# Kernel optimization log

Measured on AMD Instinct MI355X. Metric: run time of the kernel, lower is better.

Reference implementation:

```python
import jax, jax.numpy as jnp
import numpy as np

B, L, H, E = 4, 2048, 8, 64
S, D = L, E

def setup_inputs() -> dict:
    key = jax.random.key(0)
    kq, kk, kv = jax.random.split(key, 3)
    queries = jax.random.normal(kq, (B, L, H, E), dtype=jnp.float32)
    keys = jax.random.normal(kk, (B, S, H, E), dtype=jnp.float32)
    values = jax.random.normal(kv, (B, S, H, D), dtype=jnp.float32)
    # TriangularCausalMask: True above the diagonal -> masked out
    attn_mask = jnp.broadcast_to(
        jnp.triu(jnp.ones((L, S), dtype=bool), k=1)[None, None], (B, 1, L, S)
    )
    return {"queries": queries, "keys": keys, "values": values, "attn_mask": attn_mask}

def reference(queries, keys, values, attn_mask):
    E_ = queries.shape[-1]
    scale = 1.0 / jnp.sqrt(jnp.float32(E_))
    # scores: [B, H, L, S]
    scores = jnp.einsum('blhe,bshe->bhls', queries, keys)
    scores = jnp.where(attn_mask, -jnp.inf, scores)
    A = jax.nn.softmax(scale * scores, axis=-1)  # dropout p=0.01 omitted (eval/deterministic)
    V = jnp.einsum('bhls,bshd->blhd', A, values)
    return (V, A)
```

## Files before the change

kernel.cpp:

```cpp
#include <hip/hip_runtime.h>
#include <hip/hip_bf16.h>
#include <stdint.h>
#include <stddef.h>

typedef __bf16 bf16;
typedef __attribute__((ext_vector_type(8))) __bf16 bf16x8;
typedef __attribute__((ext_vector_type(4))) float f32x4;
typedef unsigned short u16;
typedef __attribute__((ext_vector_type(4))) u16 u16x4;

#define NB 4
#define NL 2048
#define NH 8
#define NE 64
#define NS 2048
#define ND 64
#define CM 0.18033688011112042f
#define STR 72

__device__ __forceinline__ void barrier_keep_vm() {
    asm volatile("s_waitcnt lgkmcnt(0)" ::: "memory");
    __builtin_amdgcn_s_barrier();
    asm volatile("" ::: "memory");
}

__global__ __launch_bounds__(512, 4)
void attn_fwd(const float* __restrict__ Qg, const float* __restrict__ Kg,
              const float* __restrict__ Vg, float* __restrict__ Og,
              float* __restrict__ Ag)
{
    __shared__ __attribute__((aligned(16))) bf16 Kl[2][64 * STR];
    __shared__ __attribute__((aligned(16))) bf16 Vl[2][64 * STR];
    __shared__ __attribute__((aligned(16))) bf16 Pl[8][16 * STR];

    const int bid = blockIdx.x;
    const int x   = bid & 7;
    const int u   = bid >> 3;
    const int qb  = (u < 32) ? (u & 15) : 15 - (u & 15);
    const int bh  = x * 4 + (u >> 4);
    const int b   = bh >> 3;
    const int h   = bh & 7;
    const int q0  = qb * 128;
    const int jmax = 2 * qb + 1;

    const int tid  = threadIdx.x;
    const int wid  = tid >> 6;
    const int lane = tid & 63;
    const int g    = lane >> 4;
    const int li   = lane & 15;
    const int jd   = 2 * qb + (wid >> 2);

    const float* qp = Qg + (((size_t)b * NL + q0 + wid * 16 + li) * NH + h) * NE;
    bf16x8 qf[2];
#pragma unroll
    for (int t = 0; t < 2; ++t) {
        f32x4 x0 = *(const f32x4*)(qp + t * 32 + g * 8);
        f32x4 x1 = *(const f32x4*)(qp + t * 32 + g * 8 + 4);
        bf16x8 v;
#pragma unroll
        for (int e = 0; e < 4; ++e) { v[e] = (bf16)x0[e]; v[4 + e] = (bf16)x1[e]; }
        qf[t] = v;
    }

    float* Abase = Ag + (((size_t)(b * NH + h)) * NL + q0) * NS;

    const int srow = tid >> 3;
    const int scb  = (tid & 7) * 8;
    const float* kbase = Kg + (((size_t)b * NS + srow) * NH + h) * NE + scb;
    const float* vbase = Vg + (((size_t)b * NS + srow) * NH + h) * ND + scb;

    auto loadK = [&](int j, f32x4 r[2]) {
        const float* src = kbase + (size_t)j * 64 * NH * NE;
        r[0] = *(const f32x4*)(src);
        r[1] = *(const f32x4*)(src + 4);
    };
    auto loadV = [&](int j, f32x4 r[2]) {
        const float* src = vbase + (size_t)j * 64 * NH * ND;
        r[0] = *(const f32x4*)(src);
        r[1] = *(const f32x4*)(src + 4);
    };
    auto writeK = [&](int c, const f32x4 r[2]) {
        bf16x8 w;
#pragma unroll
        for (int e = 0; e < 4; ++e) { w[e] = (bf16)r[0][e]; w[4 + e] = (bf16)r[1][e]; }
        *(bf16x8*)(Kl[c] + srow * STR + scb) = w;
    };
    auto writeV = [&](int c, const f32x4 r[2]) {
#pragma unroll
        for (int e = 0; e < 8; ++e) {
            int d    = scb + e;
            int boff = (srow * 2) ^ (d & 48);
            *(bf16*)((char*)Vl[c] + (size_t)d * (2 * STR) + boff) = (bf16)r[e >> 2][e & 3];
        }
    };

    auto computeScores = [&](int c, int j, float sv[4][4]) {
        const bf16* kl = Kl[c];
#pragma unroll
        for (int ct = 0; ct < 4; ++ct) {
            f32x4 a = {0.f, 0.f, 0.f, 0.f};
#pragma unroll
            for (int t = 0; t < 2; ++t) {
                bf16x8 kb = *(const bf16x8*)(kl + (size_t)(ct * 16 + li) * STR + 32 * t + 8 * g);
                a = __builtin_amdgcn_mfma_f32_16x16x32_bf16(qf[t], kb, a, 0, 0, 0);
            }
            if (j == jd) {
#pragma unroll
                for (int r = 0; r < 4; ++r) {
                    int scol = j * 64 + ct * 16 + li;
                    int qrow = q0 + wid * 16 + g * 4 + r;
                    sv[ct][r] = (scol > qrow) ? -1e30f : a[r] * CM;
                }
            } else {
#pragma unroll
                for (int r = 0; r < 4; ++r) sv[ct][r] = a[r] * CM;
            }
        }
    };

    f32x4 kr[2], vr[2];
    loadK(0, kr);
    {
        f32x4 z = {0.f, 0.f, 0.f, 0.f};
        for (int j = jmax + 1; j < 32; ++j) {
            float* tb = Abase + j * 64;
#pragma unroll
            for (int s = 0; s < 4; ++s) {
                int f   = s * 512 + tid;
                int row = f >> 4;
                int c4  = (f & 15) * 4;
                __builtin_nontemporal_store(z, (f32x4*)(tb + (size_t)row * NS + c4));
            }
        }
    }

    float psum[4] = {0.f, 0.f, 0.f, 0.f};
    for (int j = 0; j <= jmax; ++j) {
        const int c = j & 1;
        writeK(c, kr);
        if (j < jmax) loadK(j + 1, kr);
        barrier_keep_vm();
        if (j <= jd) {
            float sv[4][4];
            computeScores(c, j, sv);
#pragma unroll
            for (int r = 0; r < 4; ++r) {
                float s0 = __builtin_amdgcn_exp2f(sv[0][r]) + __builtin_amdgcn_exp2f(sv[1][r]);
                float s1 = __builtin_amdgcn_exp2f(sv[2][r]) + __builtin_amdgcn_exp2f(sv[3][r]);
                psum[r] += s0 + s1;
            }
        }
    }

    loadK(0, kr);
    loadV(0, vr);

    float vinv[4];
#pragma unroll
    for (int r = 0; r < 4; ++r) {
        float s = psum[r];
#pragma unroll
        for (int mk = 1; mk < 16; mk <<= 1) s += __shfl_xor(s, mk);
        vinv[r] = 1.f / s;
    }

    f32x4 oacc[4];
#pragma unroll
    for (int dt = 0; dt < 4; ++dt) oacc[dt] = (f32x4){0.f, 0.f, 0.f, 0.f};

    barrier_keep_vm();

    for (int j = 0; j <= jmax; ++j) {
        const int c = j & 1;
        writeK(c, kr);
        writeV(c, vr);
        if (j < jmax) { loadK(j + 1, kr); loadV(j + 1, vr); }
        barrier_keep_vm();

        float* arow = Abase + (size_t)(wid * 16) * NS + j * 64;

        if (j <= jd) {
            float sv[4][4];
            computeScores(c, j, sv);

            bf16* pl = &Pl[wid][0];
#pragma unroll
            for (int ct = 0; ct < 4; ++ct)
#pragma unroll
                for (int r = 0; r < 4; ++r) {
                    float p = __builtin_amdgcn_exp2f(sv[ct][r]) * vinv[r];
                    pl[(size_t)(g * 4 + r) * STR + ct * 16 + li] = (bf16)p;
                }
            asm volatile("s_waitcnt lgkmcnt(0)" ::: "memory");
            __builtin_amdgcn_sched_barrier(0);

#pragma unroll
            for (int s = 0; s < 4; ++s) {
                int row = g + s * 4;
                u16x4 pw = *(const u16x4*)(pl + (size_t)row * STR + li * 4);
                f32x4 o;
#pragma unroll
                for (int e = 0; e < 4; ++e) {
                    uint32_t w = ((uint32_t)pw[e]) << 16;
                    o[e] = __builtin_bit_cast(float, w);
                }
                __builtin_nontemporal_store(o, (f32x4*)(arow + (size_t)row * NS + li * 4));
            }

#pragma unroll
            for (int t = 0; t < 2; ++t) {
                bf16x8 pa = *(const bf16x8*)(pl + (size_t)li * STR + 32 * t + 8 * g);
#pragma unroll
                for (int dt = 0; dt < 4; ++dt) {
                    bf16x8 vb = *(const bf16x8*)((const char*)Vl[c]
                                  + (size_t)(dt * 16 + li) * (2 * STR)
                                  + ((64 * t + 16 * g) ^ (dt * 16 & 48)));
                    oacc[dt] = __builtin_amdgcn_mfma_f32_16x16x32_bf16(pa, vb, oacc[dt], 0, 0, 0);
                }
            }
        } else {
            f32x4 z = {0.f, 0.f, 0.f, 0.f};
#pragma unroll
            for (int s = 0; s < 4; ++s) {
                int row = g + s * 4;
                __builtin_nontemporal_store(z, (f32x4*)(arow + (size_t)row * NS + li * 4));
            }
        }
    }

#pragma unroll
    for (int dt = 0; dt < 4; ++dt)
#pragma unroll
        for (int r = 0; r < 4; ++r) {
            float* op = Og + (((size_t)b * NL + q0 + wid * 16 + g * 4 + r) * NH + h) * ND
                        + dt * 16 + li;
            __builtin_nontemporal_store(oacc[dt][r], op);
        }
}

extern "C" void kernel_launch(void* const* d_in, const int* in_sizes, int n_in,
                              void* d_out, int out_size, void* d_ws, size_t ws_size,
                              hipStream_t stream) {
    (void)in_sizes; (void)n_in; (void)out_size; (void)d_ws; (void)ws_size;
    const float* Q = (const float*)d_in[0];
    const float* K = (const float*)d_in[1];
    const float* V = (const float*)d_in[2];
    float* out = (float*)d_out;
    float* Og  = out;
    float* Ag  = out + (size_t)NB * NL * NH * ND;

    attn_fwd<<<dim3(512), dim3(512), 0, stream>>>(Q, K, V, Og, Ag);
}
```

Measured before the change: 136.8 us.

## Compute row-sum pass directly from global K without LDS staging or barriers

The first softmax-denominator pass now has each wave read K tiles straight from global memory, converting them to bf16 in registers for the MFMA, instead of staging them through shared memory. Each wave also loops only up to its own diagonal tile rather than the block-wide maximum. This removes the per-tile block barriers and LDS writes from the first pass, along with the barrier before the second pass. In exchange every wave loads K redundantly from global memory or cache, and K is converted to bf16 once per wave instead of once per block.

```diff
diff --git a/kernel.cpp b/kernel.cpp
--- a/kernel.cpp
+++ b/kernel.cpp
@@ -64,62 +64,6 @@
 
     float* Abase = Ag + (((size_t)(b * NH + h)) * NL + q0) * NS;
 
-    const int srow = tid >> 3;
-    const int scb  = (tid & 7) * 8;
-    const float* kbase = Kg + (((size_t)b * NS + srow) * NH + h) * NE + scb;
-    const float* vbase = Vg + (((size_t)b * NS + srow) * NH + h) * ND + scb;
-
-    auto loadK = [&](int j, f32x4 r[2]) {
-        const float* src = kbase + (size_t)j * 64 * NH * NE;
-        r[0] = *(const f32x4*)(src);
-        r[1] = *(const f32x4*)(src + 4);
-    };
-    auto loadV = [&](int j, f32x4 r[2]) {
-        const float* src = vbase + (size_t)j * 64 * NH * ND;
-        r[0] = *(const f32x4*)(src);
-        r[1] = *(const f32x4*)(src + 4);
-    };
-    auto writeK = [&](int c, const f32x4 r[2]) {
-        bf16x8 w;
-#pragma unroll
-        for (int e = 0; e < 4; ++e) { w[e] = (bf16)r[0][e]; w[4 + e] = (bf16)r[1][e]; }
-        *(bf16x8*)(Kl[c] + srow * STR + scb) = w;
-    };
-    auto writeV = [&](int c, const f32x4 r[2]) {
-#pragma unroll
-        for (int e = 0; e < 8; ++e) {
-            int d    = scb + e;
-            int boff = (srow * 2) ^ (d & 48);
-            *(bf16*)((char*)Vl[c] + (size_t)d * (2 * STR) + boff) = (bf16)r[e >> 2][e & 3];
-        }
-    };
-
-    auto computeScores = [&](int c, int j, float sv[4][4]) {
-        const bf16* kl = Kl[c];
-#pragma unroll
-        for (int ct = 0; ct < 4; ++ct) {
-            f32x4 a = {0.f, 0.f, 0.f, 0.f};
-#pragma unroll
-            for (int t = 0; t < 2; ++t) {
-                bf16x8 kb = *(const bf16x8*)(kl + (size_t)(ct * 16 + li) * STR + 32 * t + 8 * g);
-                a = __builtin_amdgcn_mfma_f32_16x16x32_bf16(qf[t], kb, a, 0, 0, 0);
-            }
-            if (j == jd) {
-#pragma unroll
-                for (int r = 0; r < 4; ++r) {
-                    int scol = j * 64 + ct * 16 + li;
-                    int qrow = q0 + wid * 16 + g * 4 + r;
-                    sv[ct][r] = (scol > qrow) ? -1e30f : a[r] * CM;
-                }
-            } else {
-#pragma unroll
-                for (int r = 0; r < 4; ++r) sv[ct][r] = a[r] * CM;
-            }
-        }
-    };
-
-    f32x4 kr[2], vr[2];
-    loadK(0, kr);
     {
         f32x4 z = {0.f, 0.f, 0.f, 0.f};
         for (int j = jmax + 1; j < 32; ++j) {
@@ -135,14 +79,36 @@
     }
 
     float psum[4] = {0.f, 0.f, 0.f, 0.f};
-    for (int j = 0; j <= jmax; ++j) {
-        const int c = j & 1;
-        writeK(c, kr);
-        if (j < jmax) loadK(j + 1, kr);
-        barrier_keep_vm();
-        if (j <= jd) {
+    {
+        const size_t krow = (size_t)NH * NE;
+        const float* kgb  = Kg + ((size_t)b * NS * NH + h) * NE;
+        for (int j = 0; j <= jd; ++j) {
             float sv[4][4];
-            computeScores(c, j, sv);
+#pragma unroll
+            for (int ct = 0; ct < 4; ++ct) {
+                const float* kp = kgb + (size_t)(j * 64 + ct * 16 + li) * krow + 8 * g;
+                f32x4 a = {0.f, 0.f, 0.f, 0.f};
+#pragma unroll
+                for (int t = 0; t < 2; ++t) {
+                    f32x4 x0 = *(const f32x4*)(kp + 32 * t);
+                    f32x4 x1 = *(const f32x4*)(kp + 32 * t + 4);
+                    bf16x8 kb;
+#pragma unroll
+                    for (int e = 0; e < 4; ++e) { kb[e] = (bf16)x0[e]; kb[4 + e] = (bf16)x1[e]; }
+                    a = __builtin_amdgcn_mfma_f32_16x16x32_bf16(qf[t], kb, a, 0, 0, 0);
+                }
+                if (j == jd) {
+#pragma unroll
+                    for (int r = 0; r < 4; ++r) {
+                        int scol = j * 64 + ct * 16 + li;
+                        int qrow = q0 + wid * 16 + g * 4 + r;
+                        sv[ct][r] = (scol > qrow) ? -1e30f : a[r] * CM;
+                    }
+                } else {
+#pragma unroll
+                    for (int r = 0; r < 4; ++r) sv[ct][r] = a[r] * CM;
+                }
+            }
 #pragma unroll
             for (int r = 0; r < 4; ++r) {
                 float s0 = __builtin_amdgcn_exp2f(sv[0][r]) + __builtin_amdgcn_exp2f(sv[1][r]);
@@ -152,6 +118,61 @@
         }
     }
 
+    const int srow = tid >> 3;
+    const int scb  = (tid & 7) * 8;
+    const float* kbase = Kg + (((size_t)b * NS + srow) * NH + h) * NE + scb;
+    const float* vbase = Vg + (((size_t)b * NS + srow) * NH + h) * ND + scb;
+
+    auto loadK = [&](int j, f32x4 r[2]) {
+        const float* src = kbase + (size_t)j * 64 * NH * NE;
+        r[0] = *(const f32x4*)(src);
+        r[1] = *(const f32x4*)(src + 4);
+    };
+    auto loadV = [&](int j, f32x4 r[2]) {
+        const float* src = vbase + (size_t)j * 64 * NH * ND;
+        r[0] = *(const f32x4*)(src);
+        r[1] = *(const f32x4*)(src + 4);
+    };
+    auto writeK = [&](int c, const f32x4 r[2]) {
+        bf16x8 w;
+#pragma unroll
+        for (int e = 0; e < 4; ++e) { w[e] = (bf16)r[0][e]; w[4 + e] = (bf16)r[1][e]; }
+        *(bf16x8*)(Kl[c] + srow * STR + scb) = w;
+    };
+    auto writeV = [&](int c, const f32x4 r[2]) {
+#pragma unroll
+        for (int e = 0; e < 8; ++e) {
+            int d    = scb + e;
+            int boff = (srow * 2) ^ (d & 48);
+            *(bf16*)((char*)Vl[c] + (size_t)d * (2 * STR) + boff) = (bf16)r[e >> 2][e & 3];
+        }
+    };
+
+    auto computeScores = [&](int c, int j, float sv[4][4]) {
+        const bf16* kl = Kl[c];
+#pragma unroll
+        for (int ct = 0; ct < 4; ++ct) {
+            f32x4 a = {0.f, 0.f, 0.f, 0.f};
+#pragma unroll
+            for (int t = 0; t < 2; ++t) {
+                bf16x8 kb = *(const bf16x8*)(kl + (size_t)(ct * 16 + li) * STR + 32 * t + 8 * g);
+                a = __builtin_amdgcn_mfma_f32_16x16x32_bf16(qf[t], kb, a, 0, 0, 0);
+            }
+            if (j == jd) {
+#pragma unroll
+                for (int r = 0; r < 4; ++r) {
+                    int scol = j * 64 + ct * 16 + li;
+                    int qrow = q0 + wid * 16 + g * 4 + r;
+                    sv[ct][r] = (scol > qrow) ? -1e30f : a[r] * CM;
+                }
+            } else {
+#pragma unroll
+                for (int r = 0; r < 4; ++r) sv[ct][r] = a[r] * CM;
+            }
+        }
+    };
+
+    f32x4 kr[2], vr[2];
     loadK(0, kr);
     loadV(0, vr);
 
@@ -167,8 +188,6 @@
     f32x4 oacc[4];
 #pragma unroll
     for (int dt = 0; dt < 4; ++dt) oacc[dt] = (f32x4){0.f, 0.f, 0.f, 0.f};
-
-    barrier_keep_vm();
 
     for (int j = 0; j <= jmax; ++j) {
         const int c = j & 1;
```

Result: slower. 205.6 us (+50.2%).

## Process two K/V tiles per barrier in both passes and stage output through LDS

Applied to the files above, without the earlier changes.

The first pass now loads and writes two K tiles per iteration, halving the number of block barriers. The second pass keeps two K/V tile pairs in flight (tile t and tile 16+t), so each barrier covers two tiles of work and loads are issued right after each tile's compute. The attention-probability stores switch from nontemporal to regular stores, and the O output goes through an LDS scratch so it is written as 16-byte vectors. This raises register and LDS use per block, which may reduce occupancy, and the second-pass pairing gives uneven work for short rows.

```diff
diff --git a/kernel.cpp b/kernel.cpp
--- a/kernel.cpp
+++ b/kernel.cpp
@@ -17,11 +17,21 @@
 #define ND 64
 #define CM 0.18033688011112042f
 #define STR 72
+#define KBUFB (64 * STR * 2)
 
 __device__ __forceinline__ void barrier_keep_vm() {
     asm volatile("s_waitcnt lgkmcnt(0)" ::: "memory");
     __builtin_amdgcn_s_barrier();
     asm volatile("" ::: "memory");
+}
+
+__device__ __forceinline__ void block_map(int bid, int& b, int& h, int& qb) {
+    const int x  = bid & 7;
+    const int u  = bid >> 3;
+    qb = (u < 32) ? (u & 15) : 15 - (u & 15);
+    const int bh = x * 4 + (u >> 4);
+    b = bh >> 3;
+    h = bh & 7;
 }
 
 __global__ __launch_bounds__(512, 4)
@@ -29,18 +39,10 @@
               const float* __restrict__ Vg, float* __restrict__ Og,
               float* __restrict__ Ag)
 {
-    __shared__ __attribute__((aligned(16))) bf16 Kl[2][64 * STR];
-    __shared__ __attribute__((aligned(16))) bf16 Vl[2][64 * STR];
-    __shared__ __attribute__((aligned(16))) bf16 Pl[8][16 * STR];
-
-    const int bid = blockIdx.x;
-    const int x   = bid & 7;
-    const int u   = bid >> 3;
-    const int qb  = (u < 32) ? (u & 15) : 15 - (u & 15);
-    const int bh  = x * 4 + (u >> 4);
-    const int b   = bh >> 3;
-    const int h   = bh & 7;
-    const int q0  = qb * 128;
+    __shared__ __attribute__((aligned(16))) char smem[6 * KBUFB];
+
+    int b, h, qb; block_map(blockIdx.x, b, h, qb);
+    const int q0   = qb * 128;
     const int jmax = 2 * qb + 1;
 
     const int tid  = threadIdx.x;
@@ -64,62 +66,6 @@
 
     float* Abase = Ag + (((size_t)(b * NH + h)) * NL + q0) * NS;
 
-    const int srow = tid >> 3;
-    const int scb  = (tid & 7) * 8;
-    const float* kbase = Kg + (((size_t)b * NS + srow) * NH + h) * NE + scb;
-    const float* vbase = Vg + (((size_t)b * NS + srow) * NH + h) * ND + scb;
-
-    auto loadK = [&](int j, f32x4 r[2]) {
-        const float* src = kbase + (size_t)j * 64 * NH * NE;
-        r[0] = *(const f32x4*)(src);
-        r[1] = *(const f32x4*)(src + 4);
-    };
-    auto loadV = [&](int j, f32x4 r[2]) {
-        const float* src = vbase + (size_t)j * 64 * NH * ND;
-        r[0] = *(const f32x4*)(src);
-        r[1] = *(const f32x4*)(src + 4);
-    };
-    auto writeK = [&](int c, const f32x4 r[2]) {
-        bf16x8 w;
-#pragma unroll
-        for (int e = 0; e < 4; ++e) { w[e] = (bf16)r[0][e]; w[4 + e] = (bf16)r[1][e]; }
-        *(bf16x8*)(Kl[c] + srow * STR + scb) = w;
-    };
-    auto writeV = [&](int c, const f32x4 r[2]) {
-#pragma unroll
-        for (int e = 0; e < 8; ++e) {
-            int d    = scb + e;
-            int boff = (srow * 2) ^ (d & 48);
-            *(bf16*)((char*)Vl[c] + (size_t)d * (2 * STR) + boff) = (bf16)r[e >> 2][e & 3];
-        }
-    };
-
-    auto computeScores = [&](int c, int j, float sv[4][4]) {
-        const bf16* kl = Kl[c];
-#pragma unroll
-        for (int ct = 0; ct < 4; ++ct) {
-            f32x4 a = {0.f, 0.f, 0.f, 0.f};
-#pragma unroll
-            for (int t = 0; t < 2; ++t) {
-                bf16x8 kb = *(const bf16x8*)(kl + (size_t)(ct * 16 + li) * STR + 32 * t + 8 * g);
-                a = __builtin_amdgcn_mfma_f32_16x16x32_bf16(qf[t], kb, a, 0, 0, 0);
-            }
-            if (j == jd) {
-#pragma unroll
-                for (int r = 0; r < 4; ++r) {
-                    int scol = j * 64 + ct * 16 + li;
-                    int qrow = q0 + wid * 16 + g * 4 + r;
-                    sv[ct][r] = (scol > qrow) ? -1e30f : a[r] * CM;
-                }
-            } else {
-#pragma unroll
-                for (int r = 0; r < 4; ++r) sv[ct][r] = a[r] * CM;
-            }
-        }
-    };
-
-    f32x4 kr[2], vr[2];
-    loadK(0, kr);
     {
         f32x4 z = {0.f, 0.f, 0.f, 0.f};
         for (int j = jmax + 1; j < 32; ++j) {
@@ -134,56 +80,116 @@
         }
     }
 
+    const int srow = tid >> 3;
+    const int scb  = (tid & 7) * 8;
+    const float* kbase = Kg + (((size_t)b * NS + srow) * NH + h) * NE + scb;
+    const float* vbase = Vg + (((size_t)b * NS + srow) * NH + h) * ND + scb;
+
+    auto loadK = [&](int j, f32x4 r[2]) {
+        const float* src = kbase + (size_t)j * 64 * NH * NE;
+        r[0] = *(const f32x4*)(src);
+        r[1] = *(const f32x4*)(src + 4);
+    };
+    auto loadV = [&](int j, f32x4 r[2]) {
+        const float* src = vbase + (size_t)j * 64 * NH * ND;
+        r[0] = *(const f32x4*)(src);
+        r[1] = *(const f32x4*)(src + 4);
+    };
+    auto writeK = [&](char* buf, const f32x4 r[2]) {
+        bf16x8 w;
+#pragma unroll
+        for (int e = 0; e < 4; ++e) { w[e] = (bf16)r[0][e]; w[4 + e] = (bf16)r[1][e]; }
+        *(bf16x8*)((bf16*)buf + srow * STR + scb) = w;
+    };
+    auto writeV = [&](char* buf, const f32x4 r[2]) {
+#pragma unroll
+        for (int e = 0; e < 8; ++e) {
+            int d    = scb + e;
+            int boff = (srow * 2) ^ (d & 48);
+            *(bf16*)(buf + (size_t)d * (2 * STR) + boff) = (bf16)r[e >> 2][e & 3];
+        }
+    };
+    auto computeScores = [&](const char* buf, int j, float sv[4][4]) {
+        const bf16* kl = (const bf16*)buf;
+#pragma unroll
+        for (int ct = 0; ct < 4; ++ct) {
+            f32x4 a = {0.f, 0.f, 0.f, 0.f};
+#pragma unroll
+            for (int t = 0; t < 2; ++t) {
+                bf16x8 kb = *(const bf16x8*)(kl + (size_t)(ct * 16 + li) * STR + 32 * t + 8 * g);
+                a = __builtin_amdgcn_mfma_f32_16x16x32_bf16(qf[t], kb, a, 0, 0, 0);
+            }
+            if (j == jd) {
+#pragma unroll
+                for (int r = 0; r < 4; ++r) {
+                    int scol = j * 64 + ct * 16 + li;
+                    int qrow = q0 + wid * 16 + g * 4 + r;
+                    sv[ct][r] = (scol > qrow) ? -1e30f : a[r] * CM;
+                }
+            } else {
+#pragma unroll
+                for (int r = 0; r < 4; ++r) sv[ct][r] = a[r] * CM;
+            }
+        }
+    };
+
     float psum[4] = {0.f, 0.f, 0.f, 0.f};
-    for (int j = 0; j <= jmax; ++j) {
-        const int c = j & 1;
-        writeK(c, kr);
-        if (j < jmax) loadK(j + 1, kr);
-        barrier_keep_vm();
+    {
+        f32x4 kr0[2], kr1[2];
+        loadK(0, kr0); loadK(1, kr1);
+        for (int jj = 0; jj <= qb; ++jj) {
+            char* buf0 = smem + ((jj & 1) * 2) * KBUFB;
+            writeK(buf0, kr0); writeK(buf0 + KBUFB, kr1);
+            if (jj < qb) { loadK(2 * jj + 2, kr0); loadK(2 * jj + 3, kr1); }
+            barrier_keep_vm();
+#pragma unroll
+            for (int t2 = 0; t2 < 2; ++t2) {
+                const int j = 2 * jj + t2;
+                if (j > jd) continue;
+                float sv[4][4];
+                computeScores(buf0 + t2 * KBUFB, j, sv);
+#pragma unroll
+                for (int r = 0; r < 4; ++r) {
+                    float s0 = __builtin_amdgcn_exp2f(sv[0][r]) + __builtin_amdgcn_exp2f(sv[1][r]);
+                    float s1 = __builtin_amdgcn_exp2f(sv[2][r]) + __builtin_amdgcn_exp2f(sv[3][r]);
+                    psum[r] += s0 + s1;
+                }
+            }
+        }
+    }
+
+    char* KA = smem;
+    char* KB = smem + KBUFB;
+    char* VA = smem + 2 * KBUFB;
+    char* VB = smem + 3 * KBUFB;
+    bf16* pl = (bf16*)(smem + 4 * KBUFB) + wid * 16 * STR;
+
+    f32x4 krA[2], vrA[2], krB[2], vrB[2];
+    loadK(0, krA); loadV(0, vrA);
+    if (16 <= jmax) { loadK(16, krB); loadV(16, vrB); }
+
+    float vinv[4];
+#pragma unroll
+    for (int r = 0; r < 4; ++r) {
+        float s = psum[r];
+#pragma unroll
+        for (int mk = 1; mk < 16; mk <<= 1) s += __shfl_xor(s, mk);
+        vinv[r] = 1.f / s;
+    }
+
+    f32x4 oacc[4];
+#pragma unroll
+    for (int dt = 0; dt < 4; ++dt) oacc[dt] = (f32x4){0.f, 0.f, 0.f, 0.f};
+
+    barrier_keep_vm();
+
+    const int NT2 = (jmax + 1 < 16) ? jmax + 1 : 16;
+
+    auto doTile = [&](const char* kbuf, const char* vbuf, int j) {
+        float* arow = Abase + (size_t)(wid * 16) * NS + j * 64;
         if (j <= jd) {
             float sv[4][4];
-            computeScores(c, j, sv);
-#pragma unroll
-            for (int r = 0; r < 4; ++r) {
-                float s0 = __builtin_amdgcn_exp2f(sv[0][r]) + __builtin_amdgcn_exp2f(sv[1][r]);
-                float s1 = __builtin_amdgcn_exp2f(sv[2][r]) + __builtin_amdgcn_exp2f(sv[3][r]);
-                psum[r] += s0 + s1;
-            }
-        }
-    }
-
-    loadK(0, kr);
-    loadV(0, vr);
-
-    float vinv[4];
-#pragma unroll
-    for (int r = 0; r < 4; ++r) {
-        float s = psum[r];
-#pragma unroll
-        for (int mk = 1; mk < 16; mk <<= 1) s += __shfl_xor(s, mk);
-        vinv[r] = 1.f / s;
-    }
-
-    f32x4 oacc[4];
-#pragma unroll
-    for (int dt = 0; dt < 4; ++dt) oacc[dt] = (f32x4){0.f, 0.f, 0.f, 0.f};
-
-    barrier_keep_vm();
-
-    for (int j = 0; j <= jmax; ++j) {
-        const int c = j & 1;
-        writeK(c, kr);
-        writeV(c, vr);
-        if (j < jmax) { loadK(j + 1, kr); loadV(j + 1, vr); }
-        barrier_keep_vm();
-
-        float* arow = Abase + (size_t)(wid * 16) * NS + j * 64;
-
-        if (j <= jd) {
-            float sv[4][4];
-            computeScores(c, j, sv);
-
-            bf16* pl = &Pl[wid][0];
+            computeScores(kbuf, j, sv);
 #pragma unroll
             for (int ct = 0; ct < 4; ++ct)
 #pragma unroll
@@ -204,15 +210,14 @@
                     uint32_t w = ((uint32_t)pw[e]) << 16;
                     o[e] = __builtin_bit_cast(float, w);
                 }
-                __builtin_nontemporal_store(o, (f32x4*)(arow + (size_t)row * NS + li * 4));
-            }
-
+                *(f32x4*)(arow + (size_t)row * NS + li * 4) = o;
+            }
 #pragma unroll
             for (int t = 0; t < 2; ++t) {
                 bf16x8 pa = *(const bf16x8*)(pl + (size_t)li * STR + 32 * t + 8 * g);
 #pragma unroll
                 for (int dt = 0; dt < 4; ++dt) {
-                    bf16x8 vb = *(const bf16x8*)((const char*)Vl[c]
+                    bf16x8 vb = *(const bf16x8*)(vbuf
                                   + (size_t)(dt * 16 + li) * (2 * STR)
                                   + ((64 * t + 16 * g) ^ (dt * 16 & 48)));
                     oacc[dt] = __builtin_amdgcn_mfma_f32_16x16x32_bf16(pa, vb, oacc[dt], 0, 0, 0);
@@ -223,19 +228,41 @@
 #pragma unroll
             for (int s = 0; s < 4; ++s) {
                 int row = g + s * 4;
-                __builtin_nontemporal_store(z, (f32x4*)(arow + (size_t)row * NS + li * 4));
-            }
-        }
-    }
-
+                *(f32x4*)(arow + (size_t)row * NS + li * 4) = z;
+            }
+        }
+    };
+
+    for (int t = 0; t < NT2; ++t) {
+        const bool stagedB = (16 + t <= jmax);
+        writeK(KA, krA); writeV(VA, vrA);
+        if (stagedB) { writeK(KB, krB); writeV(VB, vrB); }
+        barrier_keep_vm();
+
+        doTile(KA, VA, t);
+        if (t + 1 < NT2) { loadK(t + 1, krA); loadV(t + 1, vrA); }
+        if (stagedB) {
+            doTile(KB, VB, 16 + t);
+            if (16 + t + 1 <= jmax) { loadK(17 + t, krB); loadV(17 + t, vrB); }
+        }
+        barrier_keep_vm();
+    }
+
+    float* scr = (float*)smem + wid * 1024;
 #pragma unroll
     for (int dt = 0; dt < 4; ++dt)
 #pragma unroll
-        for (int r = 0; r < 4; ++r) {
-            float* op = Og + (((size_t)b * NL + q0 + wid * 16 + g * 4 + r) * NH + h) * ND
-                        + dt * 16 + li;
-            __builtin_nontemporal_store(oacc[dt][r], op);
-        }
+        for (int r = 0; r < 4; ++r)
+            scr[(g * 4 + r) * 64 + dt * 16 + li] = oacc[dt][r];
+    asm volatile("s_waitcnt lgkmcnt(0)" ::: "memory");
+    __builtin_amdgcn_sched_barrier(0);
+#pragma unroll
+    for (int s = 0; s < 4; ++s) {
+        int row = g + s * 4;
+        f32x4 o = *(const f32x4*)(scr + row * 64 + li * 4);
+        float* op = Og + (((size_t)b * NL + q0 + wid * 16 + row) * NH + h) * ND + li * 4;
+        __builtin_nontemporal_store(o, (f32x4*)op);
+    }
 }
 
 extern "C" void kernel_launch(void* const* d_in, const int* in_sizes, int n_in,
```

Measured after the change: 161.5 us. 1.18x slower.
